# Performance work log

Measured on AMD Instinct MI355X. Metric: run time of the kernel, lower is better.

The kernel has to match this reference:

```python
import jax, jax.numpy as jnp
import numpy as np
import itertools

ZOOM = 2.0  # zoom_factor per init_kwargs


def _interpn_linear(vol, locs):
    """vol: [*vol_shape, C]; locs: list of nb_dims float arrays of shape new_shape."""
    nb = len(locs)
    C = vol.shape[-1]
    max_loc = [vol.shape[d] - 1 for d in range(nb)]
    clipped = [jnp.clip(locs[d], 0.0, max_loc[d]) for d in range(nb)]
    loc0 = [jnp.clip(jnp.floor(locs[d]), 0.0, max_loc[d]) for d in range(nb)]
    loc1 = [jnp.clip(loc0[d] + 1.0, 0.0, max_loc[d]) for d in range(nb)]
    i0 = [x.astype(jnp.int32) for x in loc0]
    i1 = [x.astype(jnp.int32) for x in loc1]
    diff1 = [loc1[d] - clipped[d] for d in range(nb)]  # weight paired with corner 0
    diff0 = [1.0 - diff1[d] for d in range(nb)]        # weight paired with corner 1
    idxs = [i0, i1]
    wts = [diff1, diff0]
    volf = vol.reshape(-1, C)
    # column-major-style flattening per sub2ind: k = cumprod(reversed vol_shape)
    k = np.cumprod(np.array(vol.shape[:-1])[::-1])
    out = jnp.zeros(locs[0].shape + (C,), dtype=vol.dtype)
    for c in itertools.product([0, 1], repeat=nb):  # 2^nb corners (fixed, small)
        subs = [idxs[c[d]][d] for d in range(nb)]
        flat = subs[-1]
        for i, v in enumerate(subs[:-1][::-1]):
            flat = flat + v * int(k[i])
        val = volf[flat]  # gather -> [*new_shape, C]
        w = wts[c[0]][0]
        for d in range(1, nb):
            w = w * wts[c[d]][d]
        out = out + w[..., None] * val
    return out


def _resize_one(vol):
    """vol: [D,H,W,C] -> [2D,2H,2W,C] via linear interp at loc = grid/zoom."""
    nb = vol.ndim - 1
    new_shape = tuple(int(vol.shape[d] * ZOOM) for d in range(nb))
    grids = jnp.meshgrid(*[jnp.arange(n, dtype=jnp.float32) for n in new_shape],
                         indexing='ij')
    locs = [g / ZOOM for g in grids]  # grid + offset, offset = grid/zoom - grid
    return _interpn_linear(vol, locs)


def setup_inputs() -> dict:
    key = jax.random.key(0)
    vol = jax.random.normal(key, (2, 96, 96, 96, 2), dtype=jnp.float32)
    return {"vol": vol}


def reference(vol):
    return jax.vmap(_resize_one)(vol)  # [B, 192, 192, 192, 2]
```

## Files before the change

### kernel.cpp

```cpp
#include <hip/hip_runtime.h>

constexpr int NIN = 96, NOUT = 192;
constexpr int TZ = 2, TY = 4;
constexpr int HZ = TZ + 1, HY = TY + 1;
constexpr int ROWS = HZ * HY;
constexpr int HXP = 98;
constexpr int F4R = NIN / 2;
constexpr int NTZ = NIN / TZ, NTY = NIN / TY;
constexpr int NBLK = 2 * NTZ * NTY;
constexpr int NXCD = 8;
constexpr int CPX = NBLK / NXCD;

typedef float vfloat4 __attribute__((ext_vector_type(4)));

__global__ __launch_bounds__(192) void resize_zoom2_v4(
        const float* __restrict__ in, float* __restrict__ out) {
    __shared__ __align__(16) float2 S[ROWS * HXP];

    const int bid0 = blockIdx.x;
    const int bid  = (bid0 & (NXCD - 1)) * CPX + (bid0 >> 3);

    const int yt = bid % NTY;
    const int tt = bid / NTY;
    const int zt = tt % NTZ;
    const int b  = tt / NTZ;
    const int z0 = zt * TZ, y0 = yt * TY;

    const float* vb = in + (size_t)b * ((size_t)NIN * NIN * NIN * 2);
    const float4* vin4 = (const float4*)vb;

    if (threadIdx.x < ROWS) {
        int r = threadIdx.x;
        int zi = min(z0 + r / HY, NIN - 1);
        int yi = min(y0 + r % HY, NIN - 1);
        S[r * HXP + NIN] = ((const float2*)vb)[(size_t)(zi * NIN + yi) * NIN + (NIN - 1)];
    }
    for (int i = threadIdx.x; i < ROWS * F4R; i += 192) {
        int r = i / F4R, col = i - r * F4R;
        int zi = min(z0 + r / HY, NIN - 1);
        int yi = min(y0 + (r - (r / HY) * HY), NIN - 1);
        float4 v = vin4[(size_t)(zi * NIN + yi) * F4R + col];
        *(float4*)((float*)(S + r * HXP) + 4 * col) = v;
    }
    __syncthreads();

    const int xp = threadIdx.x % NIN;
    const int yh = threadIdx.x / NIN;
    vfloat4* vout = (vfloat4*)out;
    constexpr size_t ZSTR = (size_t)NOUT * (NOUT / 2);
    size_t ob = ((size_t)(b * NOUT + 2 * z0) * NOUT + (2 * y0 + yh)) * (NOUT / 2) + xp;

    #pragma unroll
    for (int y2 = 0; y2 < TY; ++y2) {
        const int yo = 2 * y2 + yh;
        const int yA = yo >> 1, yB = yA + (yo & 1);
        const float2* pA = S + yA * HXP;
        const float2* pB = S + yB * HXP;

        float2 aA = pA[xp],     aB = pB[xp];
        float2 cA = pA[xp + 1], cB = pB[xp + 1];
        float sy_x  = aA.x + aB.x, sy_y  = aA.y + aB.y;
        float syc_x = cA.x + cB.x, syc_y = cA.y + cB.y;
        size_t o = ob + (size_t)y2 * NOUT;

        #pragma unroll
        for (int k = 0; k < TZ; ++k) {
            const float2* qA = pA + (k + 1) * HY * HXP;
            const float2* qB = pB + (k + 1) * HY * HXP;
            float2 bA = qA[xp],     bB = qB[xp];
            float2 dA = qA[xp + 1], dB = qB[xp + 1];
            float ty_x  = bA.x + bB.x, ty_y  = bA.y + bB.y;
            float tyc_x = dA.x + dB.x, tyc_y = dA.y + dB.y;

            vfloat4 e0 = { 0.5f * sy_x, 0.5f * sy_y,
                           0.25f * (sy_x + syc_x), 0.25f * (sy_y + syc_y) };
            __builtin_nontemporal_store(e0, &vout[o + (size_t)(2 * k) * ZSTR]);
            float ux = sy_x + ty_x, uy = sy_y + ty_y;
            float vx = ux + syc_x + tyc_x, vy = uy + syc_y + tyc_y;
            vfloat4 e1 = { 0.25f * ux, 0.25f * uy, 0.125f * vx, 0.125f * vy };
            __builtin_nontemporal_store(e1, &vout[o + (size_t)(2 * k + 1) * ZSTR]);

            sy_x = ty_x; sy_y = ty_y; syc_x = tyc_x; syc_y = tyc_y;
        }
    }
}

extern "C" void kernel_launch(void* const* d_in, const int* in_sizes, int n_in,
                              void* d_out, int out_size, void* d_ws, size_t ws_size,
                              hipStream_t stream) {
    const float* in = (const float*)d_in[0];
    float* out = (float*)d_out;
    const int grid = NBLK;
    resize_zoom2_v4<<<grid, 192, 0, stream>>>(in, out);
}
```

Baseline: 129.4 us.

## Assign one output z-plane per block instead of a z-tile pair

The z-tiling is restructured so that each block produces a single output z-plane for a 4-row y tile. Even planes load one input plane slab and odd planes load two. The grid grows fourfold, giving more parallelism and smaller LDS per block. In exchange, input rows are re-read more often: odd planes read two planes, so total input traffic rises and the per-block setup overhead is repeated more often.

```diff
diff --git a/kernel.cpp b/kernel.cpp
--- a/kernel.cpp
+++ b/kernel.cpp
@@ -1,45 +1,48 @@
 #include <hip/hip_runtime.h>
 
 constexpr int NIN = 96, NOUT = 192;
-constexpr int TZ = 2, TY = 4;
-constexpr int HZ = TZ + 1, HY = TY + 1;
-constexpr int ROWS = HZ * HY;
+constexpr int TY = 4;
+constexpr int HYR = TY + 1;
 constexpr int HXP = 98;
 constexpr int F4R = NIN / 2;
-constexpr int NTZ = NIN / TZ, NTY = NIN / TY;
-constexpr int NBLK = 2 * NTZ * NTY;
+constexpr int NTY = NIN / TY;
+constexpr int NBLK = 2 * NOUT * NTY;
 constexpr int NXCD = 8;
 constexpr int CPX = NBLK / NXCD;
 
 typedef float vfloat4 __attribute__((ext_vector_type(4)));
 
-__global__ __launch_bounds__(192) void resize_zoom2_v4(
+__global__ __launch_bounds__(192) void resize_zoom2_v5(
         const float* __restrict__ in, float* __restrict__ out) {
-    __shared__ __align__(16) float2 S[ROWS * HXP];
+    __shared__ __align__(16) float2 S[2 * HYR * HXP];
 
     const int bid0 = blockIdx.x;
     const int bid  = (bid0 & (NXCD - 1)) * CPX + (bid0 >> 3);
 
     const int yt = bid % NTY;
-    const int tt = bid / NTY;
-    const int zt = tt % NTZ;
-    const int b  = tt / NTZ;
-    const int z0 = zt * TZ, y0 = yt * TY;
+    const int t  = bid / NTY;
+    const int zo = t % NOUT;
+    const int b  = t / NOUT;
+    const int y0 = yt * TY;
+    const int k   = zo >> 1;
+    const int odd = zo & 1;
+    const int kp1 = min(k + 1, NIN - 1);
+    const int R   = HYR * (1 + odd);
 
     const float* vb = in + (size_t)b * ((size_t)NIN * NIN * NIN * 2);
     const float4* vin4 = (const float4*)vb;
 
-    if (threadIdx.x < ROWS) {
-        int r = threadIdx.x;
-        int zi = min(z0 + r / HY, NIN - 1);
-        int yi = min(y0 + r % HY, NIN - 1);
-        S[r * HXP + NIN] = ((const float2*)vb)[(size_t)(zi * NIN + yi) * NIN + (NIN - 1)];
+    if (threadIdx.x < R) {
+        int r  = threadIdx.x;
+        int pl = (r < HYR) ? k : kp1;
+        int yi = min(y0 + (r < HYR ? r : r - HYR), NIN - 1);
+        S[r * HXP + NIN] = ((const float2*)vb)[(size_t)(pl * NIN + yi) * NIN + (NIN - 1)];
     }
-    for (int i = threadIdx.x; i < ROWS * F4R; i += 192) {
+    for (int i = threadIdx.x; i < R * F4R; i += 192) {
         int r = i / F4R, col = i - r * F4R;
-        int zi = min(z0 + r / HY, NIN - 1);
-        int yi = min(y0 + (r - (r / HY) * HY), NIN - 1);
-        float4 v = vin4[(size_t)(zi * NIN + yi) * F4R + col];
+        int pl = (r < HYR) ? k : kp1;
+        int yi = min(y0 + (r < HYR ? r : r - HYR), NIN - 1);
+        float4 v = vin4[(size_t)(pl * NIN + yi) * F4R + col];
         *(float4*)((float*)(S + r * HXP) + 4 * col) = v;
     }
     __syncthreads();
@@ -47,40 +50,37 @@
     const int xp = threadIdx.x % NIN;
     const int yh = threadIdx.x / NIN;
     vfloat4* vout = (vfloat4*)out;
-    constexpr size_t ZSTR = (size_t)NOUT * (NOUT / 2);
-    size_t ob = ((size_t)(b * NOUT + 2 * z0) * NOUT + (2 * y0 + yh)) * (NOUT / 2) + xp;
+    size_t ob = ((size_t)(b * NOUT + zo) * NOUT + (2 * y0 + yh)) * (NOUT / 2) + xp;
 
-    #pragma unroll
-    for (int y2 = 0; y2 < TY; ++y2) {
-        const int yo = 2 * y2 + yh;
-        const int yA = yo >> 1, yB = yA + (yo & 1);
-        const float2* pA = S + yA * HXP;
-        const float2* pB = S + yB * HXP;
-
-        float2 aA = pA[xp],     aB = pB[xp];
-        float2 cA = pA[xp + 1], cB = pB[xp + 1];
-        float sy_x  = aA.x + aB.x, sy_y  = aA.y + aB.y;
-        float syc_x = cA.x + cB.x, syc_y = cA.y + cB.y;
-        size_t o = ob + (size_t)y2 * NOUT;
-
+    if (!odd) {
         #pragma unroll
-        for (int k = 0; k < TZ; ++k) {
-            const float2* qA = pA + (k + 1) * HY * HXP;
-            const float2* qB = pB + (k + 1) * HY * HXP;
-            float2 bA = qA[xp],     bB = qB[xp];
-            float2 dA = qA[xp + 1], dB = qB[xp + 1];
-            float ty_x  = bA.x + bB.x, ty_y  = bA.y + bB.y;
-            float tyc_x = dA.x + dB.x, tyc_y = dA.y + dB.y;
-
-            vfloat4 e0 = { 0.5f * sy_x, 0.5f * sy_y,
-                           0.25f * (sy_x + syc_x), 0.25f * (sy_y + syc_y) };
-            __builtin_nontemporal_store(e0, &vout[o + (size_t)(2 * k) * ZSTR]);
-            float ux = sy_x + ty_x, uy = sy_y + ty_y;
-            float vx = ux + syc_x + tyc_x, vy = uy + syc_y + tyc_y;
-            vfloat4 e1 = { 0.25f * ux, 0.25f * uy, 0.125f * vx, 0.125f * vy };
-            __builtin_nontemporal_store(e1, &vout[o + (size_t)(2 * k + 1) * ZSTR]);
-
-            sy_x = ty_x; sy_y = ty_y; syc_x = tyc_x; syc_y = tyc_y;
+        for (int y2 = 0; y2 < TY; ++y2) {
+            int yo = 2 * y2 + yh;
+            int yA = yo >> 1, yB = yA + (yo & 1);
+            float2 aA = S[yA * HXP + xp],     aB = S[yB * HXP + xp];
+            float2 cA = S[yA * HXP + xp + 1], cB = S[yB * HXP + xp + 1];
+            float sx  = aA.x + aB.x, sy  = aA.y + aB.y;
+            float scx = cA.x + cB.x, scy = cA.y + cB.y;
+            vfloat4 e = { 0.5f * sx, 0.5f * sy,
+                          0.25f * (sx + scx), 0.25f * (sy + scy) };
+            __builtin_nontemporal_store(e, &vout[ob + (size_t)y2 * NOUT]);
+        }
+    } else {
+        #pragma unroll
+        for (int y2 = 0; y2 < TY; ++y2) {
+            int yo = 2 * y2 + yh;
+            int yA = yo >> 1, yB = yA + (yo & 1);
+            float2 aA = S[yA * HXP + xp],           aB = S[yB * HXP + xp];
+            float2 cA = S[yA * HXP + xp + 1],       cB = S[yB * HXP + xp + 1];
+            float2 bA = S[(HYR + yA) * HXP + xp],   bB = S[(HYR + yB) * HXP + xp];
+            float2 dA = S[(HYR + yA) * HXP + xp + 1], dB = S[(HYR + yB) * HXP + xp + 1];
+            float ux = aA.x + aB.x + bA.x + bB.x;
+            float uy = aA.y + aB.y + bA.y + bB.y;
+            float vx = ux + cA.x + cB.x + dA.x + dB.x;
+            float vy = uy + cA.y + cB.y + dA.y + dB.y;
+            vfloat4 e = { 0.25f * ux, 0.25f * uy,
+                          0.125f * vx, 0.125f * vy };
+            __builtin_nontemporal_store(e, &vout[ob + (size_t)y2 * NOUT]);
         }
     }
 }
@@ -90,6 +90,5 @@
                               hipStream_t stream) {
     const float* in = (const float*)d_in[0];
     float* out = (float*)d_out;
-    const int grid = NBLK;
-    resize_zoom2_v4<<<grid, 192, 0, stream>>>(in, out);
+    resize_zoom2_v5<<<NBLK, 192, 0, stream>>>(in, out);
 }
```

Measured after the change: 132.8 us. 2.6% more time.
